# Optimization experiments

Measured on AMD Instinct MI355X. Metric: run time of the kernel, lower is better.

## Reference

```python
import jax, jax.numpy as jnp
import numpy as np

B, N, N_HEAD, HDIM = 16, 512, 8, 64


def setup_inputs() -> dict:
    key = jax.random.key(0)
    kq, kk, kv, kg = jax.random.split(key, 4)
    q = jax.random.normal(kq, (B, N, N_HEAD, HDIM), dtype=jnp.float32)
    k = jax.random.normal(kk, (B, N, N_HEAD, HDIM), dtype=jnp.float32)
    v = jax.random.normal(kv, (B, N, N_HEAD, HDIM), dtype=jnp.float32)
    geo_f = jax.random.normal(kg, (B, N, N), dtype=jnp.float32)
    return {"q": q, "k": k, "v": v, "geo_f": geo_f}


def reference(q, k, v, geo_f):
    # q,k,v: [B,N,H,D]; geo_f: [B,N,N]
    D = q.shape[-1]
    scale = D ** (-0.5)  # total_weight = qk_weight / scale  (i.e. * sqrt(D))
    # pairwise_distance = negative squared Euclidean distance between per-head
    # query/key vectors: -||q_i - k_j||^2 = 2 q.k - ||q||^2 - ||k||^2
    qk = jnp.einsum('bnhd,bmhd->bhnm', q, k)            # [B,H,N,N]
    q2 = jnp.sum(q * q, axis=-1).transpose(0, 2, 1)     # [B,H,N]
    k2 = jnp.sum(k * k, axis=-1).transpose(0, 2, 1)     # [B,H,N]
    dist = 2.0 * qk - q2[..., :, None] - k2[..., None, :]
    total = (dist + geo_f[:, None, :, :]) / scale       # geo bias broadcast over heads
    # global max subtraction in the source is a no-op under softmax; softmax is stable anyway
    w = jax.nn.softmax(total, axis=-1)                  # [B,H,N,N]
    # weighted sum over keys m (dropout p=0.0 -> identity)
    out = jnp.einsum('bmhd,bhnm->bnhd', v, w)           # [B,N,H,D]
    return out
```

## Files before the change

kernel.cpp:

```cpp
#include <hip/hip_runtime.h>
#include <hip/hip_bf16.h>

#define BB 16
#define NN 512
#define NH 8
#define DD 64
#define QBLK 64
#define WAVES 4
#define CK 64
#define NCH 8
#define TL 4
#define KBLK 128
#define NCHUNK 4
#define NT 32
#define TPC 8

typedef __attribute__((ext_vector_type(8))) short bf16x8;
typedef __attribute__((ext_vector_type(4))) float f32x4;

__device__ __forceinline__ unsigned short f2bf(float f) {
    unsigned int u = __float_as_uint(f);
    u += 0x7fffu + ((u >> 16) & 1u);
    return (unsigned short)(u >> 16);
}
__device__ __forceinline__ float bf2f(unsigned short h) {
    return __uint_as_float(((unsigned int)h) << 16);
}
__device__ __forceinline__ void gload16(const void* gsrc, void* lds) {
    __builtin_amdgcn_global_load_lds(
        (const __attribute__((address_space(1))) unsigned int*)gsrc,
        (__attribute__((address_space(3))) unsigned int*)lds, 16, 0, 0);
}

__global__ __launch_bounds__(256) void geo_prep(
    const float* __restrict__ K, const float* __restrict__ V,
    unsigned short* __restrict__ KhiG, unsigned short* __restrict__ KloG,
    unsigned short* __restrict__ VtG, float* __restrict__ k2G)
{
    const int c2 = blockIdx.x;
    const int h  = blockIdx.y;
    const int b  = blockIdx.z;
    const int bh = b*NH + h;
    const int tid = threadIdx.x;
    const int lane16 = tid & 15;
    const int grp    = tid >> 4;

    __shared__ unsigned short Vl[DD*66];

    const size_t kbase = (size_t)bh*(NN*DD) + (size_t)c2*(CK*DD);
    #pragma unroll
    for (int kk = 0; kk < 4; ++kk) {
        const int kl = kk*16 + grp;
        const float* krow = K + ((size_t)(((b*NN + c2*CK + kl)*NH) + h))*DD + lane16*4;
        const float* vrow = V + ((size_t)(((b*NN + c2*CK + kl)*NH) + h))*DD + lane16*4;
        float4 kf = *(const float4*)krow;
        float4 vf = *(const float4*)vrow;
        float fb[4] = {kf.x, kf.y, kf.z, kf.w};
        float vb[4] = {vf.x, vf.y, vf.z, vf.w};
        unsigned short hu[4], lu[4];
        float k2s = 0.f;
        #pragma unroll
        for (int e = 0; e < 4; ++e) {
            float f = fb[e];
            k2s += f*f;
            hu[e] = f2bf(f);
            lu[e] = f2bf(f - bf2f(hu[e]));
            Vl[(lane16*4 + e)*66 + kl] = f2bf(vb[e]);
        }
        k2s += __shfl_xor(k2s, 1);
        k2s += __shfl_xor(k2s, 2);
        k2s += __shfl_xor(k2s, 4);
        k2s += __shfl_xor(k2s, 8);
        if (lane16 == 0) k2G[bh*NN + c2*CK + kl] = k2s;
        const int pos = (kl*DD + lane16*4) ^ ((kl & 7) << 3);
        *(uint2*)&KhiG[kbase + pos] = make_uint2((unsigned)hu[0] | ((unsigned)hu[1] << 16),
                                                 (unsigned)hu[2] | ((unsigned)hu[3] << 16));
        *(uint2*)&KloG[kbase + pos] = make_uint2((unsigned)lu[0] | ((unsigned)lu[1] << 16),
                                                 (unsigned)lu[2] | ((unsigned)lu[3] << 16));
    }
    __syncthreads();
    const size_t vbase = ((size_t)bh*NCH + c2)*(DD*CK);
    #pragma unroll
    for (int i = 0; i < 4; ++i) {
        const int gi = tid + 256*i;
        const int d   = gi >> 4;
        const int kl4 = (gi & 15) * 4;
        unsigned short e0 = Vl[d*66 + kl4+0];
        unsigned short e1 = Vl[d*66 + kl4+1];
        unsigned short e2 = Vl[d*66 + kl4+2];
        unsigned short e3 = Vl[d*66 + kl4+3];
        const int pos = (d*CK + kl4) ^ ((d & 7) << 3);
        *(uint2*)&VtG[vbase + pos] = make_uint2((unsigned)e0 | ((unsigned)e1 << 16),
                                                (unsigned)e2 | ((unsigned)e3 << 16));
    }
}

__global__ __launch_bounds__(256, 3) void geo_attn_main(
    const float* __restrict__ Q, const float* __restrict__ GEO,
    const unsigned short* __restrict__ KhiG, const unsigned short* __restrict__ KloG,
    const unsigned short* __restrict__ VtG, const float* __restrict__ k2G,
    float* __restrict__ OUT)
{
    const int qt  = blockIdx.x;
    const int h   = blockIdx.y;
    const int b   = blockIdx.z;
    const int bh  = b*NH + h;
    const int tid = threadIdx.x;
    const int w    = tid >> 6;
    const int lane = tid & 63;
    const int g = lane >> 4;
    const int c = lane & 15;

    __shared__ unsigned short Khi[CK*DD];
    __shared__ unsigned short Klo[CK*DD];
    __shared__ unsigned short vT [DD*CK];
    __shared__ float geoS[QBLK*CK];
    __shared__ unsigned short Pld[WAVES*16*CK];
    __shared__ float k2s[NN];
    __shared__ float sRow[WAVES][16];
    __shared__ float rowinv[WAVES][16];

    if (tid < 128) *(float4*)&k2s[tid*4] = *(const float4*)&k2G[(size_t)bh*NN + tid*4];

    const int qb = qt*QBLK + w*16;

    bf16x8 qhi[2], qlo[2];
    float q2v = 0.f;
    {
        const float* qrow = Q + ((size_t)((b*NN + qb + c)*NH + h))*DD;
        #pragma unroll
        for (int dc = 0; dc < 2; ++dc) {
            float buf[8];
            *(float4*)&buf[0] = *(const float4*)(qrow + dc*32 + g*8);
            *(float4*)&buf[4] = *(const float4*)(qrow + dc*32 + g*8 + 4);
            #pragma unroll
            for (int i = 0; i < 8; ++i) {
                float f = buf[i];
                q2v += f*f;
                unsigned short hu = f2bf(f);
                qhi[dc][i] = (short)hu;
                qlo[dc][i] = (short)f2bf(f - bf2f(hu));
            }
        }
    }
    q2v += __shfl_xor(q2v, 16);
    q2v += __shfl_xor(q2v, 32);
    float nq2[4];
    #pragma unroll
    for (int r = 0; r < 4; ++r) nq2[r] = -8.f * __shfl(q2v, g*4 + r);

    f32x4 oacc[4];
    #pragma unroll
    for (int cb = 0; cb < 4; ++cb) { oacc[cb][0]=0.f; oacc[cb][1]=0.f; oacc[cb][2]=0.f; oacc[cb][3]=0.f; }
    float m_r[4] = {-3e38f, -3e38f, -3e38f, -3e38f};
    float l_r[4] = {0.f, 0.f, 0.f, 0.f};

    const char* gKhiB = (const char*)KhiG + (size_t)bh*(NN*DD*2);
    const char* gKloB = (const char*)KloG + (size_t)bh*(NN*DD*2);
    const char* gVtB  = (const char*)VtG  + (size_t)bh*(NN*DD*2);
    const float* geoQ = GEO + (size_t)b*NN*NN + (size_t)(qt*QBLK)*NN;

    for (int ch = 0; ch < NCH; ++ch) {
        __syncthreads();
        {
            const char* srcKhi = gKhiB + ch*(CK*DD*2);
            const char* srcKlo = gKloB + ch*(CK*DD*2);
            const char* srcVt  = gVtB  + ch*(CK*DD*2);
            #pragma unroll
            for (int i = 0; i < 2; ++i) {
                const int off = (w*2 + i)*1024;
                gload16(srcKhi + off + (lane<<4), (char*)Khi + off);
                gload16(srcKlo + off + (lane<<4), (char*)Klo + off);
                gload16(srcVt  + off + (lane<<4), (char*)vT  + off);
            }
            #pragma unroll
            for (int i = 0; i < 4; ++i) {
                const int seg = w*4 + i;
                const int row = seg*4 + (lane >> 4);
                const int cg  = (lane & 15) ^ (row & 7);
                gload16((const void*)(geoQ + (size_t)row*NN + ch*CK + cg*4),
                        (char*)geoS + seg*1024);
            }
        }
        __syncthreads();

        f32x4 sacc[TL];
        #pragma unroll
        for (int tl = 0; tl < TL; ++tl) { sacc[tl][0]=0.f; sacc[tl][1]=0.f; sacc[tl][2]=0.f; sacc[tl][3]=0.f; }
        #pragma unroll
        for (int tl = 0; tl < TL; ++tl) {
            const int key = tl*16 + c;
            #pragma unroll
            for (int dc = 0; dc < 2; ++dc) {
                const int idx = (key*DD + dc*32 + g*8) ^ ((key & 7) << 3);
                bf16x8 kh = *(const bf16x8*)&Khi[idx];
                bf16x8 kl = *(const bf16x8*)&Klo[idx];
                sacc[tl] = __builtin_amdgcn_mfma_f32_16x16x32_bf16(qhi[dc], kh, sacc[tl], 0,0,0);
                sacc[tl] = __builtin_amdgcn_mfma_f32_16x16x32_bf16(qlo[dc], kh, sacc[tl], 0,0,0);
                sacc[tl] = __builtin_amdgcn_mfma_f32_16x16x32_bf16(qhi[dc], kl, sacc[tl], 0,0,0);
            }
        }

        const int row_base = w*16 + 4*g;
        float cmax[4] = {-3e38f, -3e38f, -3e38f, -3e38f};
        #pragma unroll
        for (int tl = 0; tl < TL; ++tl) {
            const float kk8 = -8.f * k2s[ch*CK + tl*16 + c];
            #pragma unroll
            for (int r = 0; r < 4; ++r) {
                const int rl = row_base + r;
                const float gv = geoS[(rl*16 + ((tl*4 + (c>>2)) ^ (rl & 7)))*4 + (c & 3)];
                float s = fmaf(16.f, sacc[tl][r], fmaf(8.f, gv, nq2[r] + kk8));
                sacc[tl][r] = s;
                cmax[r] = fmaxf(cmax[r], s);
            }
        }
        float fac[4];
        #pragma unroll
        for (int r = 0; r < 4; ++r) {
            float mv = cmax[r];
            mv = fmaxf(mv, __shfl_xor(mv, 1));
            mv = fmaxf(mv, __shfl_xor(mv, 2));
            mv = fmaxf(mv, __shfl_xor(mv, 4));
            mv = fmaxf(mv, __shfl_xor(mv, 8));
            const float mnew = fmaxf(m_r[r], mv);
            fac[r] = __expf(m_r[r] - mnew);
            m_r[r] = mnew;
        }
        if (c == 0) {
            #pragma unroll
            for (int r = 0; r < 4; ++r) sRow[w][4*g + r] = fac[r];
        }
        #pragma unroll
        for (int r = 0; r < 4; ++r) l_r[r] *= fac[r];
        #pragma unroll
        for (int tl = 0; tl < TL; ++tl) {
            #pragma unroll
            for (int r = 0; r < 4; ++r) {
                float p = __expf(sacc[tl][r] - m_r[r]);
                l_r[r] += p;
                const int qloc = 4*g + r;
                Pld[(((w*16 + qloc)*CK) + tl*16 + c) ^ ((qloc & 7) << 3)] = f2bf(p);
            }
        }
        __syncthreads();

        const float sc = sRow[w][c];
        #pragma unroll
        for (int cb = 0; cb < 4; ++cb) {
            oacc[cb][0] *= sc; oacc[cb][1] *= sc; oacc[cb][2] *= sc; oacc[cb][3] *= sc;
        }
        #pragma unroll
        for (int kc = 0; kc < 2; ++kc) {
            bf16x8 pf = *(const bf16x8*)&Pld[(((w*16 + c)*CK) + kc*32 + g*8) ^ ((c & 7) << 3)];
            #pragma unroll
            for (int cb = 0; cb < 4; ++cb) {
                const int d = cb*16 + c;
                bf16x8 vfr = *(const bf16x8*)&vT[(d*CK + kc*32 + g*8) ^ ((d & 7) << 3)];
                oacc[cb] = __builtin_amdgcn_mfma_f32_16x16x32_bf16(vfr, pf, oacc[cb], 0,0,0);
            }
        }
    }

    #pragma unroll
    for (int r = 0; r < 4; ++r) {
        float sv = l_r[r];
        sv += __shfl_xor(sv, 1);
        sv += __shfl_xor(sv, 2);
        sv += __shfl_xor(sv, 4);
        sv += __shfl_xor(sv, 8);
        if (c == 0) rowinv[w][4*g + r] = 1.f / sv;
    }
    __syncthreads();
    const float inv = rowinv[w][c];
    float* orow = OUT + ((size_t)((b*NN + qb + c)*NH + h))*DD + 4*g;
    #pragma unroll
    for (int cb = 0; cb < 4; ++cb) {
        float4 ov;
        ov.x = oacc[cb][0] * inv;
        ov.y = oacc[cb][1] * inv;
        ov.z = oacc[cb][2] * inv;
        ov.w = oacc[cb][3] * inv;
        *(float4*)(orow + cb*16) = ov;
    }
}

__global__ __launch_bounds__(256, 2) void geo_attn_fallback(
    const float* __restrict__ Q, const float* __restrict__ K,
    const float* __restrict__ V, const float* __restrict__ GEO,
    float* __restrict__ OUT)
{
    const int qt  = blockIdx.x;
    const int h   = blockIdx.y;
    const int b   = blockIdx.z;
    const int tid = threadIdx.x;
    const int w    = tid >> 6;
    const int lane = tid & 63;
    const int g = lane >> 4;
    const int c = lane & 15;

    __shared__ unsigned short smemA[16384];
    __shared__ float k2p[2][NN];
    __shared__ float rowinvF[WAVES][16];

    unsigned short* KhiF = smemA;
    unsigned short* KloF = smemA + KBLK*DD;
    unsigned short* vTF  = smemA;
    unsigned short* PldF = smemA + DD*KBLK + w*16*KBLK;

    const int qb = qt*QBLK + w*16;

    bf16x8 qhi[2], qlo[2];
    float q2v = 0.f;
    {
        const float* qrow = Q + ((size_t)((b*NN + qb + c)*NH + h))*DD;
        #pragma unroll
        for (int dc = 0; dc < 2; ++dc) {
            float buf[8];
            *(float4*)&buf[0] = *(const float4*)(qrow + dc*32 + g*8);
            *(float4*)&buf[4] = *(const float4*)(qrow + dc*32 + g*8 + 4);
            #pragma unroll
            for (int i = 0; i < 8; ++i) {
                float f = buf[i];
                q2v += f*f;
                unsigned short hu = f2bf(f);
                qhi[dc][i] = (short)hu;
                qlo[dc][i] = (short)f2bf(f - bf2f(hu));
            }
        }
    }
    q2v += __shfl_xor(q2v, 16);
    q2v += __shfl_xor(q2v, 32);

    f32x4 zero4; zero4[0]=0.f; zero4[1]=0.f; zero4[2]=0.f; zero4[3]=0.f;
    f32x4 acc[NT];
    #pragma unroll
    for (int t = 0; t < NT; ++t) acc[t] = zero4;

    #pragma unroll
    for (int c2 = 0; c2 < NCHUNK; ++c2) {
        __syncthreads();
        {
            const int keyl = tid & (KBLK-1);
            const int half = tid >> 7;
            const int d0 = half*32;
            const float* krow = K + ((size_t)((b*NN + c2*KBLK + keyl)*NH + h))*DD + d0;
            float k2sv = 0.f;
            #pragma unroll
            for (int jj = 0; jj < 8; ++jj) {
                float4 f4 = *(const float4*)(krow + jj*4);
                float fb[4] = {f4.x, f4.y, f4.z, f4.w};
                unsigned short hu[4], lu[4];
                #pragma unroll
                for (int e = 0; e < 4; ++e) {
                    float f = fb[e];
                    k2sv += f*f;
                    hu[e] = f2bf(f);
                    lu[e] = f2bf(f - bf2f(hu[e]));
                }
                int idx = (keyl*DD + d0 + jj*4) ^ ((keyl & 7) << 3);
                *(uint2*)&KhiF[idx] = make_uint2((unsigned)hu[0] | ((unsigned)hu[1] << 16),
                                                 (unsigned)hu[2] | ((unsigned)hu[3] << 16));
                *(uint2*)&KloF[idx] = make_uint2((unsigned)lu[0] | ((unsigned)lu[1] << 16),
                                                 (unsigned)lu[2] | ((unsigned)lu[3] << 16));
            }
            k2p[half][c2*KBLK + keyl] = k2sv;
        }
        __syncthreads();
        #pragma unroll
        for (int tl = 0; tl < TPC; ++tl) {
            const int key = tl*16 + c;
            #pragma unroll
            for (int dc = 0; dc < 2; ++dc) {
                int idx = (key*DD + dc*32 + g*8) ^ ((key & 7) << 3);
                bf16x8 kh = *(const bf16x8*)&KhiF[idx];
                bf16x8 kl = *(const bf16x8*)&KloF[idx];
                acc[c2*TPC+tl] = __builtin_amdgcn_mfma_f32_16x16x32_bf16(qhi[dc], kh, acc[c2*TPC+tl], 0,0,0);
                acc[c2*TPC+tl] = __builtin_amdgcn_mfma_f32_16x16x32_bf16(qlo[dc], kh, acc[c2*TPC+tl], 0,0,0);
                acc[c2*TPC+tl] = __builtin_amdgcn_mfma_f32_16x16x32_bf16(qhi[dc], kl, acc[c2*TPC+tl], 0,0,0);
            }
        }
    }

    float nq2[4];
    #pragma unroll
    for (int r = 0; r < 4; ++r) nq2[r] = -8.f * __shfl(q2v, g*4 + r);

    const float* geoB = GEO + (size_t)b*NN*NN + (size_t)(qb + 4*g)*NN;

    float mx[4] = {-3e38f, -3e38f, -3e38f, -3e38f};
    #pragma unroll
    for (int t = 0; t < NT; ++t) {
        float kk8 = -8.f * (k2p[0][t*16 + c] + k2p[1][t*16 + c]);
        #pragma unroll
        for (int r = 0; r < 4; ++r) {
            float gv = geoB[(size_t)r*NN + t*16 + c];
            float s = fmaf(16.f, acc[t][r], fmaf(8.f, gv, nq2[r] + kk8));
            acc[t][r] = s;
            mx[r] = fmaxf(mx[r], s);
        }
    }
    #pragma unroll
    for (int r = 0; r < 4; ++r) {
        float mv = mx[r];
        mv = fmaxf(mv, __shfl_xor(mv, 1));
        mv = fmaxf(mv, __shfl_xor(mv, 2));
        mv = fmaxf(mv, __shfl_xor(mv, 4));
        mv = fmaxf(mv, __shfl_xor(mv, 8));
        mx[r] = mv;
    }
    float sm[4] = {0.f, 0.f, 0.f, 0.f};
    #pragma unroll
    for (int t = 0; t < NT; ++t) {
        #pragma unroll
        for (int r = 0; r < 4; ++r) {
            float p = __expf(acc[t][r] - mx[r]);
            acc[t][r] = p;
            sm[r] += p;
        }
    }
    #pragma unroll
    for (int r = 0; r < 4; ++r) {
        float sv = sm[r];
        sv += __shfl_xor(sv, 1);
        sv += __shfl_xor(sv, 2);
        sv += __shfl_xor(sv, 4);
        sv += __shfl_xor(sv, 8);
        sm[r] = sv;
    }
    if (c == 0) {
        #pragma unroll
        for (int r = 0; r < 4; ++r) rowinvF[w][4*g + r] = 1.f / sm[r];
    }

    f32x4 oacc[4];
    #pragma unroll
    for (int cb = 0; cb < 4; ++cb) oacc[cb] = zero4;

    #pragma unroll
    for (int c2 = 0; c2 < NCHUNK; ++c2) {
        __syncthreads();
        {
            const int keyl = tid & (KBLK-1);
            const int half = tid >> 7;
            const int d0 = half*32;
            const float* vrow = V + ((size_t)((b*NN + c2*KBLK + keyl)*NH + h))*DD + d0;
            #pragma unroll
            for (int jj = 0; jj < 8; ++jj) {
                float4 f4 = *(const float4*)(vrow + jj*4);
                float fb[4] = {f4.x, f4.y, f4.z, f4.w};
                #pragma unroll
                for (int e = 0; e < 4; ++e) {
                    int d = d0 + jj*4 + e;
                    vTF[(d*KBLK + keyl) ^ ((d & 7) << 3)] = f2bf(fb[e]);
                }
            }
        }
        #pragma unroll
        for (int tl = 0; tl < TPC; ++tl) {
            #pragma unroll
            for (int r = 0; r < 4; ++r) {
                int qloc = 4*g + r;
                PldF[(qloc*KBLK + tl*16 + c) ^ ((qloc & 7) << 3)] = f2bf(acc[c2*TPC+tl][r]);
            }
        }
        __syncthreads();
        #pragma unroll
        for (int kc = 0; kc < 4; ++kc) {
            int kb2 = kc*32 + g*8;
            bf16x8 pf = *(const bf16x8*)&PldF[(c*KBLK + kb2) ^ ((c & 7) << 3)];
            #pragma unroll
            for (int cb = 0; cb < 4; ++cb) {
                int d = cb*16 + c;
                bf16x8 vf = *(const bf16x8*)&vTF[(d*KBLK + kb2) ^ ((d & 7) << 3)];
                oacc[cb] = __builtin_amdgcn_mfma_f32_16x16x32_bf16(vf, pf, oacc[cb], 0,0,0);
            }
        }
    }

    const float inv = rowinvF[w][c];
    float* orow = OUT + ((size_t)((b*NN + qb + c)*NH + h))*DD + 4*g;
    #pragma unroll
    for (int cb = 0; cb < 4; ++cb) {
        float4 ov;
        ov.x = oacc[cb][0] * inv;
        ov.y = oacc[cb][1] * inv;
        ov.z = oacc[cb][2] * inv;
        ov.w = oacc[cb][3] * inv;
        *(float4*)(orow + cb*16) = ov;
    }
}

extern "C" void kernel_launch(void* const* d_in, const int* in_sizes, int n_in,
                              void* d_out, int out_size, void* d_ws, size_t ws_size,
                              hipStream_t stream) {
    const float* q   = (const float*)d_in[0];
    const float* k   = (const float*)d_in[1];
    const float* v   = (const float*)d_in[2];
    const float* geo = (const float*)d_in[3];
    float* out = (float*)d_out;

    const size_t IMG = (size_t)BB*NH*NN*DD*2;
    const size_t need = 3*IMG + (size_t)BB*NH*NN*4;

    if (ws_size >= need) {
        unsigned short* KhiG = (unsigned short*)d_ws;
        unsigned short* KloG = (unsigned short*)((char*)d_ws + IMG);
        unsigned short* VtG  = (unsigned short*)((char*)d_ws + 2*IMG);
        float*          k2G  = (float*)((char*)d_ws + 3*IMG);
        dim3 pgrid(NCH, NH, BB);
        geo_prep<<<pgrid, 256, 0, stream>>>(k, v, KhiG, KloG, VtG, k2G);
        dim3 grid(NN/QBLK, NH, BB);
        geo_attn_main<<<grid, 256, 0, stream>>>(q, geo, KhiG, KloG, VtG, k2G, out);
    } else {
        dim3 grid(NN/QBLK, NH, BB);
        geo_attn_fallback<<<grid, 256, 0, stream>>>(q, k, v, geo, out);
    }
}
```

Measured before the change: 154.4 us.

## Double-buffer K/V chunks, widen blocks to 8 waves, load geo bias directly to registers

The main attention kernel now uses 512-thread blocks covering 128 query rows, so each staged K/V chunk is shared by twice as many waves. K-hi, K-lo and V-transposed chunks are double-buffered in LDS, so the next chunk loads while the current one is computed. The geo bias is read from global memory straight into registers rather than staged through LDS. The change also adds s_setprio around the MFMA sections and remaps block IDs so that blocks sharing a batch/head are spread in a specific order. In exchange, register pressure rises from the per-thread geo loads, and the uncoalesced strided geo reads may cost bandwidth.

```diff
diff --git a/kernel.cpp b/kernel.cpp
--- a/kernel.cpp
+++ b/kernel.cpp
@@ -5,11 +5,13 @@
 #define NN 512
 #define NH 8
 #define DD 64
-#define QBLK 64
-#define WAVES 4
 #define CK 64
 #define NCH 8
 #define TL 4
+#define MWAVES 8
+#define MQBLK 128
+#define QBLK 64
+#define WAVES 4
 #define KBLK 128
 #define NCHUNK 4
 #define NT 32
@@ -95,34 +97,35 @@
     }
 }
 
-__global__ __launch_bounds__(256, 3) void geo_attn_main(
+__global__ __launch_bounds__(512, 4) void geo_attn_main(
     const float* __restrict__ Q, const float* __restrict__ GEO,
     const unsigned short* __restrict__ KhiG, const unsigned short* __restrict__ KloG,
     const unsigned short* __restrict__ VtG, const float* __restrict__ k2G,
     float* __restrict__ OUT)
 {
-    const int qt  = blockIdx.x;
-    const int h   = blockIdx.y;
-    const int b   = blockIdx.z;
-    const int bh  = b*NH + h;
+    const int bid  = blockIdx.x;
+    const int tile = (bid & 7) * 64 + (bid >> 3);
+    const int qt = tile & 3;
+    const int h  = (tile >> 2) & 7;
+    const int b  = tile >> 5;
+    const int bh = b*NH + h;
     const int tid = threadIdx.x;
     const int w    = tid >> 6;
     const int lane = tid & 63;
     const int g = lane >> 4;
     const int c = lane & 15;
 
-    __shared__ unsigned short Khi[CK*DD];
-    __shared__ unsigned short Klo[CK*DD];
-    __shared__ unsigned short vT [DD*CK];
-    __shared__ float geoS[QBLK*CK];
-    __shared__ unsigned short Pld[WAVES*16*CK];
+    __shared__ unsigned short Khi[2][CK*DD];
+    __shared__ unsigned short Klo[2][CK*DD];
+    __shared__ unsigned short vT [2][CK*DD];
+    __shared__ unsigned short Pld[MWAVES*16*CK];
     __shared__ float k2s[NN];
-    __shared__ float sRow[WAVES][16];
-    __shared__ float rowinv[WAVES][16];
-
-    if (tid < 128) *(float4*)&k2s[tid*4] = *(const float4*)&k2G[(size_t)bh*NN + tid*4];
-
-    const int qb = qt*QBLK + w*16;
+    __shared__ float sRow[MWAVES][16];
+    __shared__ float rowinv[MWAVES][16];
+
+    if (tid < NN) k2s[tid] = k2G[(size_t)bh*NN + tid];
+
+    const int qb = qt*MQBLK + w*16;
 
     bf16x8 qhi[2], qlo[2];
     float q2v = 0.f;
@@ -158,59 +161,57 @@
     const char* gKhiB = (const char*)KhiG + (size_t)bh*(NN*DD*2);
     const char* gKloB = (const char*)KloG + (size_t)bh*(NN*DD*2);
     const char* gVtB  = (const char*)VtG  + (size_t)bh*(NN*DD*2);
-    const float* geoQ = GEO + (size_t)b*NN*NN + (size_t)(qt*QBLK)*NN;
+
+    auto stage = [&](int buf, int ch2) {
+        const int off = w*1024 + (lane<<4);
+        gload16(gKhiB + ch2*(CK*DD*2) + off, (char*)&Khi[buf][0] + w*1024);
+        gload16(gKloB + ch2*(CK*DD*2) + off, (char*)&Klo[buf][0] + w*1024);
+        gload16(gVtB  + ch2*(CK*DD*2) + off, (char*)&vT [buf][0] + w*1024);
+    };
+
+    stage(0, 0);
+    __syncthreads();
 
     for (int ch = 0; ch < NCH; ++ch) {
-        __syncthreads();
+        const int cur = ch & 1;
+        if (ch + 1 < NCH) stage(cur ^ 1, ch + 1);
+
+        float greg[16];
         {
-            const char* srcKhi = gKhiB + ch*(CK*DD*2);
-            const char* srcKlo = gKloB + ch*(CK*DD*2);
-            const char* srcVt  = gVtB  + ch*(CK*DD*2);
-            #pragma unroll
-            for (int i = 0; i < 2; ++i) {
-                const int off = (w*2 + i)*1024;
-                gload16(srcKhi + off + (lane<<4), (char*)Khi + off);
-                gload16(srcKlo + off + (lane<<4), (char*)Klo + off);
-                gload16(srcVt  + off + (lane<<4), (char*)vT  + off);
-            }
-            #pragma unroll
-            for (int i = 0; i < 4; ++i) {
-                const int seg = w*4 + i;
-                const int row = seg*4 + (lane >> 4);
-                const int cg  = (lane & 15) ^ (row & 7);
-                gload16((const void*)(geoQ + (size_t)row*NN + ch*CK + cg*4),
-                        (char*)geoS + seg*1024);
-            }
-        }
-        __syncthreads();
+            const float* gb2 = GEO + (size_t)b*NN*NN + (size_t)(qb + 4*g)*NN + ch*CK + c;
+            #pragma unroll
+            for (int tl = 0; tl < TL; ++tl)
+                #pragma unroll
+                for (int r = 0; r < 4; ++r)
+                    greg[tl*4+r] = gb2[(size_t)r*NN + tl*16];
+        }
 
         f32x4 sacc[TL];
         #pragma unroll
         for (int tl = 0; tl < TL; ++tl) { sacc[tl][0]=0.f; sacc[tl][1]=0.f; sacc[tl][2]=0.f; sacc[tl][3]=0.f; }
+        __builtin_amdgcn_s_setprio(1);
         #pragma unroll
         for (int tl = 0; tl < TL; ++tl) {
             const int key = tl*16 + c;
             #pragma unroll
             for (int dc = 0; dc < 2; ++dc) {
                 const int idx = (key*DD + dc*32 + g*8) ^ ((key & 7) << 3);
-                bf16x8 kh = *(const bf16x8*)&Khi[idx];
-                bf16x8 kl = *(const bf16x8*)&Klo[idx];
+                bf16x8 kh = *(const bf16x8*)&Khi[cur][idx];
+                bf16x8 kl = *(const bf16x8*)&Klo[cur][idx];
                 sacc[tl] = __builtin_amdgcn_mfma_f32_16x16x32_bf16(qhi[dc], kh, sacc[tl], 0,0,0);
                 sacc[tl] = __builtin_amdgcn_mfma_f32_16x16x32_bf16(qlo[dc], kh, sacc[tl], 0,0,0);
                 sacc[tl] = __builtin_amdgcn_mfma_f32_16x16x32_bf16(qhi[dc], kl, sacc[tl], 0,0,0);
             }
         }
-
-        const int row_base = w*16 + 4*g;
+        __builtin_amdgcn_s_setprio(0);
+
         float cmax[4] = {-3e38f, -3e38f, -3e38f, -3e38f};
         #pragma unroll
         for (int tl = 0; tl < TL; ++tl) {
             const float kk8 = -8.f * k2s[ch*CK + tl*16 + c];
             #pragma unroll
             for (int r = 0; r < 4; ++r) {
-                const int rl = row_base + r;
-                const float gv = geoS[(rl*16 + ((tl*4 + (c>>2)) ^ (rl & 7)))*4 + (c & 3)];
-                float s = fmaf(16.f, sacc[tl][r], fmaf(8.f, gv, nq2[r] + kk8));
+                float s = fmaf(16.f, sacc[tl][r], fmaf(8.f, greg[tl*4+r], nq2[r] + kk8));
                 sacc[tl][r] = s;
                 cmax[r] = fmaxf(cmax[r], s);
             }
@@ -250,16 +251,19 @@
         for (int cb = 0; cb < 4; ++cb) {
             oacc[cb][0] *= sc; oacc[cb][1] *= sc; oacc[cb][2] *= sc; oacc[cb][3] *= sc;
         }
+        __builtin_amdgcn_s_setprio(1);
         #pragma unroll
         for (int kc = 0; kc < 2; ++kc) {
             bf16x8 pf = *(const bf16x8*)&Pld[(((w*16 + c)*CK) + kc*32 + g*8) ^ ((c & 7) << 3)];
             #pragma unroll
             for (int cb = 0; cb < 4; ++cb) {
                 const int d = cb*16 + c;
-                bf16x8 vfr = *(const bf16x8*)&vT[(d*CK + kc*32 + g*8) ^ ((d & 7) << 3)];
+                bf16x8 vfr = *(const bf16x8*)&vT[cur][(d*CK + kc*32 + g*8) ^ ((d & 7) << 3)];
                 oacc[cb] = __builtin_amdgcn_mfma_f32_16x16x32_bf16(vfr, pf, oacc[cb], 0,0,0);
             }
         }
+        __builtin_amdgcn_s_setprio(0);
+        __syncthreads();
     }
 
     #pragma unroll
@@ -510,8 +514,7 @@
         float*          k2G  = (float*)((char*)d_ws + 3*IMG);
         dim3 pgrid(NCH, NH, BB);
         geo_prep<<<pgrid, 256, 0, stream>>>(k, v, KhiG, KloG, VtG, k2G);
-        dim3 grid(NN/QBLK, NH, BB);
-        geo_attn_main<<<grid, 256, 0, stream>>>(q, geo, KhiG, KloG, VtG, k2G, out);
+        geo_attn_main<<<dim3(512), 512, 0, stream>>>(q, geo, KhiG, KloG, VtG, k2G, out);
     } else {
         dim3 grid(NN/QBLK, NH, BB);
         geo_attn_fallback<<<grid, 256, 0, stream>>>(q, k, v, geo, out);
```

Measured after the change: 144.1 us. 6.7% less time.
